# Optimization experiments

Measured on AMD Instinct MI355X. Metric: run time of the kernel, lower is better.

## Reference

```python
import jax, jax.numpy as jnp
import numpy as np

N, F_IN, D_OUT, H = 8192, 512, 64, 8
ALPHA = 0.2
NEG_INF = jnp.float32(-9e15)


def setup_inputs() -> dict:
    key = jax.random.key(0)
    k1, k2, k3, k4, k5 = jax.random.split(key, 5)
    x = jax.random.normal(k1, (N, F_IN), dtype=jnp.float32)
    # sparse-ish binary adjacency (avg degree ~33) with self-loops, stored dense
    adj = (jax.random.uniform(k2, (N, N)) < 0.004).astype(jnp.float32)
    adj = jnp.maximum(adj, jnp.eye(N, dtype=jnp.float32))
    W = jax.random.normal(k3, (H, F_IN, D_OUT), dtype=jnp.float32) * 0.05
    a1 = jax.random.normal(k4, (H, D_OUT), dtype=jnp.float32) * 0.05
    a2 = jax.random.normal(k5, (H, D_OUT), dtype=jnp.float32) * 0.05
    return {"x": x, "adj": adj, "W": W, "a1": a1, "a2": a2}


def reference(x, adj, W, a1, a2):
    mask = adj > 0
    outputs = []
    for h in range(H):  # fixed small head count (matches original per-head loop)
        Wh = x @ W[h]                      # [N, D]
        f1 = Wh @ a1[h]                    # [N]
        f2 = Wh @ a2[h]                    # [N]
        e = jax.nn.leaky_relu(f1[:, None] + f2[None, :], ALPHA)  # [N, N]
        att = jnp.where(mask, e, NEG_INF)
        att = jax.nn.softmax(att, axis=1)  # dropout omitted (eval mode)
        outputs.append(att @ Wh)           # [N, D]
    return jnp.concatenate(outputs, axis=1)  # [N, H*D]
```

## Files before the change

kernel.cpp:

```cpp
#include <hip/hip_runtime.h>
#include <hip/hip_bf16.h>
#include <cstdint>

#define N_NODES 8192
#define F_IN    512
#define D_O     64
#define H_N     8
#define NOUT    512
#define MAXD    128

#define BM 64
#define BN 128
#define BK 64

typedef __attribute__((ext_vector_type(8))) short short8;
typedef __attribute__((ext_vector_type(4))) float f32x4;

static __device__ __forceinline__ ushort f2bf(float f) {
  union { float f; uint32_t u; } v; v.f = f;
  uint32_t r = v.u + 0x7FFFu + ((v.u >> 16) & 1u);
  return (ushort)(r >> 16);
}
static __device__ __forceinline__ float bf2f(ushort u) {
  union { uint32_t u; float f; } v; v.u = ((uint32_t)u) << 16;
  return v.f;
}

__global__ __launch_bounds__(256) void convert(const float* __restrict__ x,
                                               const float* __restrict__ W,
                                               ushort* __restrict__ xb,
                                               ushort* __restrict__ Wt) {
  __shared__ float Ws[64][65];
  const int b = blockIdx.x, t = threadIdx.x;
  if (b < 2048) {
    const int gid = b * 256 + t;
    #pragma unroll
    for (int it = 0; it < 2; ++it) {
      const int q = gid + it * 524288;
      const float4 v = ((const float4*)x)[q];
      ushort4 u;
      u.x = f2bf(v.x); u.y = f2bf(v.y); u.z = f2bf(v.z); u.w = f2bf(v.w);
      ((ushort4*)xb)[q] = u;
    }
  } else {
    const int bb = b - 2048;
    const int h = bb >> 3, kt = bb & 7;
    const int d = t & 63, krg = (t >> 6) * 16;
    const float* src = &W[((size_t)h * F_IN + kt * 64 + krg) * D_O + d];
    #pragma unroll
    for (int q = 0; q < 16; ++q)
      Ws[krg + q][d] = src[(size_t)q * D_O];
    __syncthreads();
    const int d0 = t >> 2, kq = (t & 3) * 16;
    ushort* dst = &Wt[(size_t)h * D_O * F_IN + (size_t)d0 * F_IN + kt * 64 + kq];
    #pragma unroll
    for (int q = 0; q < 16; ++q)
      dst[q] = f2bf(Ws[kq + q][d0]);
  }
}

__global__ __launch_bounds__(256) void scan_gemm(const uint32_t* __restrict__ adj,
                                                 const ushort* __restrict__ xb,
                                                 const ushort* __restrict__ Wt,
                                                 const float* __restrict__ a1,
                                                 const float* __restrict__ a2,
                                                 ushort* __restrict__ Whb,
                                                 float* __restrict__ f1,
                                                 float* __restrict__ f2,
                                                 int* __restrict__ nbr_g,
                                                 int* __restrict__ deg_g) {
  __shared__ ushort As[BM][BK + 8];
  __shared__ ushort Bs[BN][BK + 8];
  __shared__ int wsum[4];

  const int id   = blockIdx.x;
  const int tid  = threadIdx.x;
  const int lane = tid & 63;
  const int wv   = tid >> 6;

  if (id < 512) {
    const int wr = wv >> 1, wc = wv & 1;
    const int r0 = (id >> 2) * BM;
    const int c0 = (id & 3) * BN;
    const int lm = lane & 15;
    const int lg = lane >> 4;

    f32x4 acc[2][4];
    #pragma unroll
    for (int m2 = 0; m2 < 2; ++m2)
      #pragma unroll
      for (int n2 = 0; n2 < 4; ++n2)
        acc[m2][n2] = (f32x4){0.f, 0.f, 0.f, 0.f};

    for (int k0 = 0; k0 < F_IN; k0 += BK) {
      __syncthreads();
      #pragma unroll
      for (int p = 0; p < 2; ++p) {
        const int e = p * 256 + tid;
        const int row = e >> 3, ck = (e & 7) * 8;
        *(short8*)&As[row][ck] = *(const short8*)&xb[(size_t)(r0 + row) * F_IN + k0 + ck];
      }
      #pragma unroll
      for (int p = 0; p < 4; ++p) {
        const int e = p * 256 + tid;
        const int row = e >> 3, ck = (e & 7) * 8;
        *(short8*)&Bs[row][ck] = *(const short8*)&Wt[(size_t)(c0 + row) * F_IN + k0 + ck];
      }
      __syncthreads();

      #pragma unroll
      for (int kk = 0; kk < 2; ++kk) {
        const int koff = kk * 32 + lg * 8;
        short8 af[2], bf[4];
        #pragma unroll
        for (int m2 = 0; m2 < 2; ++m2)
          af[m2] = *(const short8*)&As[wr * 32 + m2 * 16 + lm][koff];
        #pragma unroll
        for (int n2 = 0; n2 < 4; ++n2)
          bf[n2] = *(const short8*)&Bs[wc * 64 + n2 * 16 + lm][koff];
        #pragma unroll
        for (int m2 = 0; m2 < 2; ++m2)
          #pragma unroll
          for (int n2 = 0; n2 < 4; ++n2)
            acc[m2][n2] = __builtin_amdgcn_mfma_f32_16x16x32_bf16(af[m2], bf[n2], acc[m2][n2], 0, 0, 0);
      }
    }

    const int head = (c0 >> 6) + wc;
    float a1v[4], a2v[4];
    #pragma unroll
    for (int n2 = 0; n2 < 4; ++n2) {
      a1v[n2] = a1[head * D_O + n2 * 16 + lm];
      a2v[n2] = a2[head * D_O + n2 * 16 + lm];
    }
    #pragma unroll
    for (int m2 = 0; m2 < 2; ++m2) {
      #pragma unroll
      for (int r = 0; r < 4; ++r) {
        const int row = r0 + wr * 32 + m2 * 16 + lg * 4 + r;
        float p1 = 0.f, p2 = 0.f;
        #pragma unroll
        for (int n2 = 0; n2 < 4; ++n2) {
          const float v = acc[m2][n2][r];
          p1 += v * a1v[n2];
          p2 += v * a2v[n2];
          Whb[(size_t)row * NOUT + c0 + wc * 64 + n2 * 16 + lm] = f2bf(v);
        }
        #pragma unroll
        for (int o = 1; o < 16; o <<= 1) {
          p1 += __shfl_xor(p1, o);
          p2 += __shfl_xor(p2, o);
        }
        if (lm == 0) {
          f1[(size_t)row * H_N + head] = p1;
          f2[(size_t)row * H_N + head] = p2;
        }
      }
    }
  } else {
    const int i = id - 512;
    const uint32_t* arow = adj + (size_t)i * N_NODES;
    uint32_t bits = 0;
    #pragma unroll
    for (int u = 0; u < 8; ++u) {
      const uint4 a = *(const uint4*)&arow[(u * 256 + tid) * 4];
      if (a.x) bits |= 1u << (u * 4 + 0);
      if (a.y) bits |= 1u << (u * 4 + 1);
      if (a.z) bits |= 1u << (u * 4 + 2);
      if (a.w) bits |= 1u << (u * 4 + 3);
    }
    const int cnt = __popc(bits);
    int v = cnt;
    #pragma unroll
    for (int o = 1; o < 64; o <<= 1) {
      int u = __shfl_up(v, o);
      if (lane >= o) v += u;
    }
    if (lane == 63) wsum[wv] = v;
    __syncthreads();
    int base = 0, total = 0;
    #pragma unroll
    for (int ww = 0; ww < 4; ++ww) {
      int s = wsum[ww];
      if (ww < wv) base += s;
      total += s;
    }
    int off = base + v - cnt;
    #pragma unroll
    for (int u = 0; u < 8; ++u)
      #pragma unroll
      for (int bq = 0; bq < 4; ++bq)
        if (bits & (1u << (u * 4 + bq))) {
          if (off < MAXD) nbr_g[(size_t)i * MAXD + off] = (u * 256 + tid) * 4 + bq;
          ++off;
        }
    if (tid == 0) deg_g[i] = min(total, MAXD);
  }
}

__global__ __launch_bounds__(64) void gat_panel(const int* __restrict__ nbr_g,
                                                const int* __restrict__ deg_g,
                                                const ushort* __restrict__ Whb,
                                                const float* __restrict__ f1,
                                                const float* __restrict__ f2,
                                                float* __restrict__ out) {
  const int bid = blockIdx.x;
  const int P   = bid >> 13;
  const int i   = bid & 8191;
  const int t   = threadIdx.x;

  __shared__ int   nbr[MAXD];
  __shared__ float ff[MAXD][2];
  __shared__ float ps[MAXD][2];
  __shared__ float f1s2[2], invs2[2];

  const int deg = deg_g[i];
  if (t < deg)      nbr[t]      = nbr_g[(size_t)i * MAXD + t];
  if (t + 64 < deg) nbr[t + 64] = nbr_g[(size_t)i * MAXD + t + 64];
  if (t < 2) f1s2[t] = f1[(size_t)i * H_N + 2 * P + t];
  __syncthreads();

  for (int n = t; n < deg; n += 64) {
    const float2 v = *(const float2*)&f2[(size_t)nbr[n] * H_N + 2 * P];
    ff[n][0] = v.x; ff[n][1] = v.y;
  }
  __syncthreads();

  {
    const int h = t >> 5;
    const int l = t & 31;
    const float f1v = f1s2[h];
    float m = -3.0e38f;
    for (int n = l; n < deg; n += 32) {
      float e = f1v + ff[n][h];
      e = e > 0.f ? e : 0.2f * e;
      ps[n][h] = e;
      m = fmaxf(m, e);
    }
    #pragma unroll
    for (int o = 16; o; o >>= 1) m = fmaxf(m, __shfl_xor(m, o));
    float s = 0.f;
    for (int n = l; n < deg; n += 32) {
      const float e = __expf(ps[n][h] - m);
      ps[n][h] = e;
      s += e;
    }
    #pragma unroll
    for (int o = 16; o; o >>= 1) s += __shfl_xor(s, o);
    if (l == 0) invs2[h] = 1.0f / s;
  }
  __syncthreads();

  const int ht      = t >> 5;
  const int colbase = P * 128 + t * 2;
  float a0 = 0.f, a1c = 0.f;
  #pragma unroll 8
  for (int n = 0; n < deg; ++n) {
    const float pv = ps[n][ht];
    const ushort2 u = *(const ushort2*)&Whb[(size_t)nbr[n] * NOUT + colbase];
    a0  += pv * bf2f(u.x);
    a1c += pv * bf2f(u.y);
  }
  const float inv = invs2[ht];
  float2 o2; o2.x = a0 * inv; o2.y = a1c * inv;
  *(float2*)&out[(size_t)i * NOUT + colbase] = o2;
}

extern "C" void kernel_launch(void* const* d_in, const int* in_sizes, int n_in,
                              void* d_out, int out_size, void* d_ws, size_t ws_size,
                              hipStream_t stream) {
  const float* x   = (const float*)d_in[0];
  const float* adj = (const float*)d_in[1];
  const float* W   = (const float*)d_in[2];
  const float* a1  = (const float*)d_in[3];
  const float* a2  = (const float*)d_in[4];
  float* out = (float*)d_out;

  ushort* Whb = (ushort*)d_ws;
  ushort* xb  = Whb + (size_t)N_NODES * NOUT;
  ushort* Wt  = xb + (size_t)N_NODES * F_IN;
  float*  f1  = (float*)(Wt + (size_t)H_N * D_O * F_IN);
  float*  f2  = f1 + (size_t)N_NODES * H_N;
  int*    nbr_g = (int*)(f2 + (size_t)N_NODES * H_N);
  int*    deg_g = nbr_g + (size_t)N_NODES * MAXD;

  hipLaunchKernelGGL(convert, dim3(2112), dim3(256), 0, stream, x, W, xb, Wt);
  hipLaunchKernelGGL(scan_gemm, dim3(512 + N_NODES), dim3(256), 0, stream,
                     (const uint32_t*)adj, xb, Wt, a1, a2, Whb, f1, f2, nbr_g, deg_g);
  hipLaunchKernelGGL(gat_panel, dim3(4 * N_NODES), dim3(64), 0, stream,
                     nbr_g, deg_g, Whb, f1, f2, out);
}
```

Baseline: 94.06 us.

## Fuse x bf16 conversion into GEMM, split scan kernel, pack two rows per panel block

The standalone conversion of x to bf16 is removed. The GEMM now loads fp32 x tiles and converts them while staging into shared memory, which avoids writing and re-reading an 8 MB bf16 copy. The fused scan/GEMM kernel is split into separate scan and GEMM launches, adding one launch. The aggregation kernel now processes two rows per 128-thread block instead of one row per 64-thread block, halving the block count at the cost of some extra LDS per block.

After: 96.52 us. 2.6% more time.

```diff
diff --git a/kernel.cpp b/kernel.cpp
--- a/kernel.cpp
+++ b/kernel.cpp
@@ -26,228 +26,220 @@
   return v.f;
 }
 
-__global__ __launch_bounds__(256) void convert(const float* __restrict__ x,
-                                               const float* __restrict__ W,
-                                               ushort* __restrict__ xb,
-                                               ushort* __restrict__ Wt) {
+__global__ __launch_bounds__(256) void convert_wt(const float* __restrict__ W,
+                                                  ushort* __restrict__ Wt) {
   __shared__ float Ws[64][65];
-  const int b = blockIdx.x, t = threadIdx.x;
-  if (b < 2048) {
-    const int gid = b * 256 + t;
-    #pragma unroll
-    for (int it = 0; it < 2; ++it) {
-      const int q = gid + it * 524288;
-      const float4 v = ((const float4*)x)[q];
-      ushort4 u;
-      u.x = f2bf(v.x); u.y = f2bf(v.y); u.z = f2bf(v.z); u.w = f2bf(v.w);
-      ((ushort4*)xb)[q] = u;
-    }
-  } else {
-    const int bb = b - 2048;
-    const int h = bb >> 3, kt = bb & 7;
-    const int d = t & 63, krg = (t >> 6) * 16;
-    const float* src = &W[((size_t)h * F_IN + kt * 64 + krg) * D_O + d];
-    #pragma unroll
-    for (int q = 0; q < 16; ++q)
-      Ws[krg + q][d] = src[(size_t)q * D_O];
-    __syncthreads();
-    const int d0 = t >> 2, kq = (t & 3) * 16;
-    ushort* dst = &Wt[(size_t)h * D_O * F_IN + (size_t)d0 * F_IN + kt * 64 + kq];
-    #pragma unroll
-    for (int q = 0; q < 16; ++q)
-      dst[q] = f2bf(Ws[kq + q][d0]);
-  }
-}
-
-__global__ __launch_bounds__(256) void scan_gemm(const uint32_t* __restrict__ adj,
-                                                 const ushort* __restrict__ xb,
-                                                 const ushort* __restrict__ Wt,
-                                                 const float* __restrict__ a1,
-                                                 const float* __restrict__ a2,
-                                                 ushort* __restrict__ Whb,
-                                                 float* __restrict__ f1,
-                                                 float* __restrict__ f2,
-                                                 int* __restrict__ nbr_g,
-                                                 int* __restrict__ deg_g) {
-  __shared__ ushort As[BM][BK + 8];
-  __shared__ ushort Bs[BN][BK + 8];
+  const int bb = blockIdx.x;
+  const int t  = threadIdx.x;
+  const int h = bb >> 3, kt = bb & 7;
+  const int d = t & 63, krg = (t >> 6) * 16;
+  const float* src = &W[((size_t)h * F_IN + kt * 64 + krg) * D_O + d];
+  #pragma unroll
+  for (int q = 0; q < 16; ++q)
+    Ws[krg + q][d] = src[(size_t)q * D_O];
+  __syncthreads();
+  const int d0 = t >> 2, kq = (t & 3) * 16;
+  ushort* dst = &Wt[(size_t)h * D_O * F_IN + (size_t)d0 * F_IN + kt * 64 + kq];
+  #pragma unroll
+  for (int q = 0; q < 16; ++q)
+    dst[q] = f2bf(Ws[kq + q][d0]);
+}
+
+__global__ __launch_bounds__(256) void scan(const uint32_t* __restrict__ adj,
+                                            int* __restrict__ nbr_g,
+                                            int* __restrict__ deg_g) {
   __shared__ int wsum[4];
-
-  const int id   = blockIdx.x;
+  const int i    = blockIdx.x;
   const int tid  = threadIdx.x;
   const int lane = tid & 63;
   const int wv   = tid >> 6;
 
-  if (id < 512) {
-    const int wr = wv >> 1, wc = wv & 1;
-    const int r0 = (id >> 2) * BM;
-    const int c0 = (id & 3) * BN;
-    const int lm = lane & 15;
-    const int lg = lane >> 4;
-
-    f32x4 acc[2][4];
-    #pragma unroll
-    for (int m2 = 0; m2 < 2; ++m2)
+  const uint32_t* arow = adj + (size_t)i * N_NODES;
+  uint32_t bits = 0;
+  #pragma unroll
+  for (int u = 0; u < 8; ++u) {
+    const uint4 a = *(const uint4*)&arow[(u * 256 + tid) * 4];
+    if (a.x) bits |= 1u << (u * 4 + 0);
+    if (a.y) bits |= 1u << (u * 4 + 1);
+    if (a.z) bits |= 1u << (u * 4 + 2);
+    if (a.w) bits |= 1u << (u * 4 + 3);
+  }
+  const int cnt = __popc(bits);
+  int v = cnt;
+  #pragma unroll
+  for (int o = 1; o < 64; o <<= 1) {
+    int u = __shfl_up(v, o);
+    if (lane >= o) v += u;
+  }
+  if (lane == 63) wsum[wv] = v;
+  __syncthreads();
+  int base = 0, total = 0;
+  #pragma unroll
+  for (int ww = 0; ww < 4; ++ww) {
+    int s = wsum[ww];
+    if (ww < wv) base += s;
+    total += s;
+  }
+  int off = base + v - cnt;
+  #pragma unroll
+  for (int u = 0; u < 8; ++u)
+    #pragma unroll
+    for (int bq = 0; bq < 4; ++bq)
+      if (bits & (1u << (u * 4 + bq))) {
+        if (off < MAXD) nbr_g[(size_t)i * MAXD + off] = (u * 256 + tid) * 4 + bq;
+        ++off;
+      }
+  if (tid == 0) deg_g[i] = min(total, MAXD);
+}
+
+__global__ __launch_bounds__(256) void gemm_f(const float* __restrict__ x,
+                                              const ushort* __restrict__ Wt,
+                                              const float* __restrict__ a1,
+                                              const float* __restrict__ a2,
+                                              ushort* __restrict__ Whb,
+                                              float* __restrict__ f1,
+                                              float* __restrict__ f2) {
+  __shared__ ushort As[BM][BK + 8];
+  __shared__ ushort Bs[BN][BK + 8];
+
+  const int tid  = threadIdx.x;
+  const int lane = tid & 63;
+  const int wv   = tid >> 6;
+  const int wr   = wv >> 1, wc = wv & 1;
+  const int r0   = blockIdx.y * BM;
+  const int c0   = blockIdx.x * BN;
+  const int lm   = lane & 15;
+  const int lg   = lane >> 4;
+
+  f32x4 acc[2][4];
+  #pragma unroll
+  for (int m2 = 0; m2 < 2; ++m2)
+    #pragma unroll
+    for (int n2 = 0; n2 < 4; ++n2)
+      acc[m2][n2] = (f32x4){0.f, 0.f, 0.f, 0.f};
+
+  for (int k0 = 0; k0 < F_IN; k0 += BK) {
+    __syncthreads();
+    #pragma unroll
+    for (int p = 0; p < 4; ++p) {
+      const int e = p * 256 + tid;
+      const int row = e >> 4, q4 = (e & 15) * 4;
+      const float4 v = *(const float4*)&x[(size_t)(r0 + row) * F_IN + k0 + q4];
+      ushort4 u;
+      u.x = f2bf(v.x); u.y = f2bf(v.y); u.z = f2bf(v.z); u.w = f2bf(v.w);
+      *(ushort4*)&As[row][q4] = u;
+    }
+    #pragma unroll
+    for (int p = 0; p < 4; ++p) {
+      const int e = p * 256 + tid;
+      const int row = e >> 3, ck = (e & 7) * 8;
+      *(short8*)&Bs[row][ck] = *(const short8*)&Wt[(size_t)(c0 + row) * F_IN + k0 + ck];
+    }
+    __syncthreads();
+
+    #pragma unroll
+    for (int kk = 0; kk < 2; ++kk) {
+      const int koff = kk * 32 + lg * 8;
+      short8 af[2], bf[4];
+      #pragma unroll
+      for (int m2 = 0; m2 < 2; ++m2)
+        af[m2] = *(const short8*)&As[wr * 32 + m2 * 16 + lm][koff];
       #pragma unroll
       for (int n2 = 0; n2 < 4; ++n2)
-        acc[m2][n2] = (f32x4){0.f, 0.f, 0.f, 0.f};
-
-    for (int k0 = 0; k0 < F_IN; k0 += BK) {
-      __syncthreads();
-      #pragma unroll
-      for (int p = 0; p < 2; ++p) {
-        const int e = p * 256 + tid;
-        const int row = e >> 3, ck = (e & 7) * 8;
-        *(short8*)&As[row][ck] = *(const short8*)&xb[(size_t)(r0 + row) * F_IN + k0 + ck];
-      }
-      #pragma unroll
-      for (int p = 0; p < 4; ++p) {
-        const int e = p * 256 + tid;
-        const int row = e >> 3, ck = (e & 7) * 8;
-        *(short8*)&Bs[row][ck] = *(const short8*)&Wt[(size_t)(c0 + row) * F_IN + k0 + ck];
-      }
-      __syncthreads();
-
-      #pragma unroll
-      for (int kk = 0; kk < 2; ++kk) {
-        const int koff = kk * 32 + lg * 8;
-        short8 af[2], bf[4];
-        #pragma unroll
-        for (int m2 = 0; m2 < 2; ++m2)
-          af[m2] = *(const short8*)&As[wr * 32 + m2 * 16 + lm][koff];
+        bf[n2] = *(const short8*)&Bs[wc * 64 + n2 * 16 + lm][koff];
+      #pragma unroll
+      for (int m2 = 0; m2 < 2; ++m2)
         #pragma unroll
         for (int n2 = 0; n2 < 4; ++n2)
-          bf[n2] = *(const short8*)&Bs[wc * 64 + n2 * 16 + lm][koff];
-        #pragma unroll
-        for (int m2 = 0; m2 < 2; ++m2)
-          #pragma unroll
-          for (int n2 = 0; n2 < 4; ++n2)
-            acc[m2][n2] = __builtin_amdgcn_mfma_f32_16x16x32_bf16(af[m2], bf[n2], acc[m2][n2], 0, 0, 0);
-      }
-    }
-
-    const int head = (c0 >> 6) + wc;
-    float a1v[4], a2v[4];
-    #pragma unroll
-    for (int n2 = 0; n2 < 4; ++n2) {
-      a1v[n2] = a1[head * D_O + n2 * 16 + lm];
-      a2v[n2] = a2[head * D_O + n2 * 16 + lm];
-    }
-    #pragma unroll
-    for (int m2 = 0; m2 < 2; ++m2) {
-      #pragma unroll
-      for (int r = 0; r < 4; ++r) {
-        const int row = r0 + wr * 32 + m2 * 16 + lg * 4 + r;
-        float p1 = 0.f, p2 = 0.f;
-        #pragma unroll
-        for (int n2 = 0; n2 < 4; ++n2) {
-          const float v = acc[m2][n2][r];
-          p1 += v * a1v[n2];
-          p2 += v * a2v[n2];
-          Whb[(size_t)row * NOUT + c0 + wc * 64 + n2 * 16 + lm] = f2bf(v);
-        }
-        #pragma unroll
-        for (int o = 1; o < 16; o <<= 1) {
-          p1 += __shfl_xor(p1, o);
-          p2 += __shfl_xor(p2, o);
-        }
-        if (lm == 0) {
-          f1[(size_t)row * H_N + head] = p1;
-          f2[(size_t)row * H_N + head] = p2;
-        }
-      }
-    }
-  } else {
-    const int i = id - 512;
-    const uint32_t* arow = adj + (size_t)i * N_NODES;
-    uint32_t bits = 0;
-    #pragma unroll
-    for (int u = 0; u < 8; ++u) {
-      const uint4 a = *(const uint4*)&arow[(u * 256 + tid) * 4];
-      if (a.x) bits |= 1u << (u * 4 + 0);
-      if (a.y) bits |= 1u << (u * 4 + 1);
-      if (a.z) bits |= 1u << (u * 4 + 2);
-      if (a.w) bits |= 1u << (u * 4 + 3);
-    }
-    const int cnt = __popc(bits);
-    int v = cnt;
-    #pragma unroll
-    for (int o = 1; o < 64; o <<= 1) {
-      int u = __shfl_up(v, o);
-      if (lane >= o) v += u;
-    }
-    if (lane == 63) wsum[wv] = v;
-    __syncthreads();
-    int base = 0, total = 0;
-    #pragma unroll
-    for (int ww = 0; ww < 4; ++ww) {
-      int s = wsum[ww];
-      if (ww < wv) base += s;
-      total += s;
-    }
-    int off = base + v - cnt;
-    #pragma unroll
-    for (int u = 0; u < 8; ++u)
-      #pragma unroll
-      for (int bq = 0; bq < 4; ++bq)
-        if (bits & (1u << (u * 4 + bq))) {
-          if (off < MAXD) nbr_g[(size_t)i * MAXD + off] = (u * 256 + tid) * 4 + bq;
-          ++off;
-        }
-    if (tid == 0) deg_g[i] = min(total, MAXD);
-  }
-}
-
-__global__ __launch_bounds__(64) void gat_panel(const int* __restrict__ nbr_g,
-                                                const int* __restrict__ deg_g,
-                                                const ushort* __restrict__ Whb,
-                                                const float* __restrict__ f1,
-                                                const float* __restrict__ f2,
-                                                float* __restrict__ out) {
+          acc[m2][n2] = __builtin_amdgcn_mfma_f32_16x16x32_bf16(af[m2], bf[n2], acc[m2][n2], 0, 0, 0);
+    }
+  }
+
+  const int head = (c0 >> 6) + wc;
+  float a1v[4], a2v[4];
+  #pragma unroll
+  for (int n2 = 0; n2 < 4; ++n2) {
+    a1v[n2] = a1[head * D_O + n2 * 16 + lm];
+    a2v[n2] = a2[head * D_O + n2 * 16 + lm];
+  }
+  #pragma unroll
+  for (int m2 = 0; m2 < 2; ++m2) {
+    #pragma unroll
+    for (int r = 0; r < 4; ++r) {
+      const int row = r0 + wr * 32 + m2 * 16 + lg * 4 + r;
+      float p1 = 0.f, p2 = 0.f;
+      #pragma unroll
+      for (int n2 = 0; n2 < 4; ++n2) {
+        const float v = acc[m2][n2][r];
+        p1 += v * a1v[n2];
+        p2 += v * a2v[n2];
+        Whb[(size_t)row * NOUT + c0 + wc * 64 + n2 * 16 + lm] = f2bf(v);
+      }
+      #pragma unroll
+      for (int o = 1; o < 16; o <<= 1) {
+        p1 += __shfl_xor(p1, o);
+        p2 += __shfl_xor(p2, o);
+      }
+      if (lm == 0) {
+        f1[(size_t)row * H_N + head] = p1;
+        f2[(size_t)row * H_N + head] = p2;
+      }
+    }
+  }
+}
+
+__global__ __launch_bounds__(128) void gat_panel(const int* __restrict__ nbr_g,
+                                                 const int* __restrict__ deg_g,
+                                                 const ushort* __restrict__ Whb,
+                                                 const float* __restrict__ f1,
+                                                 const float* __restrict__ f2,
+                                                 float* __restrict__ out) {
   const int bid = blockIdx.x;
-  const int P   = bid >> 13;
-  const int i   = bid & 8191;
-  const int t   = threadIdx.x;
-
-  __shared__ int   nbr[MAXD];
-  __shared__ float ff[MAXD][2];
-  __shared__ float ps[MAXD][2];
-  __shared__ float f1s2[2], invs2[2];
+  const int P   = bid >> 12;
+  const int rp  = bid & 4095;
+  const int w   = threadIdx.x >> 6;
+  const int i   = rp * 2 + w;
+  const int t   = threadIdx.x & 63;
+
+  __shared__ int   nbr[2][MAXD];
+  __shared__ float ff[2][MAXD][2];
+  __shared__ float ps[2][MAXD][2];
+  __shared__ float f1s2[2][2], invs2[2][2];
 
   const int deg = deg_g[i];
-  if (t < deg)      nbr[t]      = nbr_g[(size_t)i * MAXD + t];
-  if (t + 64 < deg) nbr[t + 64] = nbr_g[(size_t)i * MAXD + t + 64];
-  if (t < 2) f1s2[t] = f1[(size_t)i * H_N + 2 * P + t];
+  if (t < deg)      nbr[w][t]      = nbr_g[(size_t)i * MAXD + t];
+  if (t + 64 < deg) nbr[w][t + 64] = nbr_g[(size_t)i * MAXD + t + 64];
+  if (t < 2) f1s2[w][t] = f1[(size_t)i * H_N + 2 * P + t];
   __syncthreads();
 
   for (int n = t; n < deg; n += 64) {
-    const float2 v = *(const float2*)&f2[(size_t)nbr[n] * H_N + 2 * P];
-    ff[n][0] = v.x; ff[n][1] = v.y;
+    const float2 v = *(const float2*)&f2[(size_t)nbr[w][n] * H_N + 2 * P];
+    ff[w][n][0] = v.x; ff[w][n][1] = v.y;
   }
   __syncthreads();
 
   {
     const int h = t >> 5;
     const int l = t & 31;
-    const float f1v = f1s2[h];
+    const float f1v = f1s2[w][h];
     float m = -3.0e38f;
     for (int n = l; n < deg; n += 32) {
-      float e = f1v + ff[n][h];
+      float e = f1v + ff[w][n][h];
       e = e > 0.f ? e : 0.2f * e;
-      ps[n][h] = e;
+      ps[w][n][h] = e;
       m = fmaxf(m, e);
     }
     #pragma unroll
     for (int o = 16; o; o >>= 1) m = fmaxf(m, __shfl_xor(m, o));
     float s = 0.f;
     for (int n = l; n < deg; n += 32) {
-      const float e = __expf(ps[n][h] - m);
-      ps[n][h] = e;
+      const float e = __expf(ps[w][n][h] - m);
+      ps[w][n][h] = e;
       s += e;
     }
     #pragma unroll
     for (int o = 16; o; o >>= 1) s += __shfl_xor(s, o);
-    if (l == 0) invs2[h] = 1.0f / s;
+    if (l == 0) invs2[w][h] = 1.0f / s;
   }
   __syncthreads();
 
@@ -256,12 +248,12 @@
   float a0 = 0.f, a1c = 0.f;
   #pragma unroll 8
   for (int n = 0; n < deg; ++n) {
-    const float pv = ps[n][ht];
-    const ushort2 u = *(const ushort2*)&Whb[(size_t)nbr[n] * NOUT + colbase];
+    const float pv = ps[w][n][ht];
+    const ushort2 u = *(const ushort2*)&Whb[(size_t)nbr[w][n] * NOUT + colbase];
     a0  += pv * bf2f(u.x);
     a1c += pv * bf2f(u.y);
   }
-  const float inv = invs2[ht];
+  const float inv = invs2[w][ht];
   float2 o2; o2.x = a0 * inv; o2.y = a1c * inv;
   *(float2*)&out[(size_t)i * NOUT + colbase] = o2;
 }
@@ -277,16 +269,17 @@
   float* out = (float*)d_out;
 
   ushort* Whb = (ushort*)d_ws;
-  ushort* xb  = Whb + (size_t)N_NODES * NOUT;
-  ushort* Wt  = xb + (size_t)N_NODES * F_IN;
+  ushort* Wt  = Whb + (size_t)N_NODES * NOUT;
   float*  f1  = (float*)(Wt + (size_t)H_N * D_O * F_IN);
   float*  f2  = f1 + (size_t)N_NODES * H_N;
   int*    nbr_g = (int*)(f2 + (size_t)N_NODES * H_N);
   int*    deg_g = nbr_g + (size_t)N_NODES * MAXD;
 
-  hipLaunchKernelGGL(convert, dim3(2112), dim3(256), 0, stream, x, W, xb, Wt);
-  hipLaunchKernelGGL(scan_gemm, dim3(512 + N_NODES), dim3(256), 0, stream,
-                     (const uint32_t*)adj, xb, Wt, a1, a2, Whb, f1, f2, nbr_g, deg_g);
-  hipLaunchKernelGGL(gat_panel, dim3(4 * N_NODES), dim3(64), 0, stream,
+  hipLaunchKernelGGL(convert_wt, dim3(64), dim3(256), 0, stream, W, Wt);
+  hipLaunchKernelGGL(scan, dim3(N_NODES), dim3(256), 0, stream,
+                     (const uint32_t*)adj, nbr_g, deg_g);
+  hipLaunchKernelGGL(gemm_f, dim3(NOUT / BN, N_NODES / BM), dim3(256), 0, stream,
+                     x, Wt, a1, a2, Whb, f1, f2);
+  hipLaunchKernelGGL(gat_panel, dim3(4 * N_NODES / 2), dim3(128), 0, stream,
                      nbr_g, deg_g, Whb, f1, f2, out);
 }
```

## Fuse x bf16 conversion into GEMM, merge adj scan with W convert, shrink nbr to ushort

Applied to the files above, without the earlier changes.

Drops the separate x-to-bf16 pass and its 8 MB round trip by converting x on the fly while loading A tiles in a new GEMM kernel. That kernel uses 512 threads, a 32-row tile covering all 512 output columns and a K step of 32. The adjacency scan now shares a launch with the W transpose/convert instead of the GEMM, and neighbor indices are stored as ushort to halve their traffic. The trade-off is that the GEMM now runs after the scan rather than overlapping with it, and the smaller K tile means more syncs per block.

Result: slower. 96.87 us (+3.0%).

```diff
diff --git a/kernel.cpp b/kernel.cpp
--- a/kernel.cpp
+++ b/kernel.cpp
@@ -9,9 +9,8 @@
 #define NOUT    512
 #define MAXD    128
 
-#define BM 64
-#define BN 128
-#define BK 64
+#define BM 32
+#define BK 32
 
 typedef __attribute__((ext_vector_type(8))) short short8;
 typedef __attribute__((ext_vector_type(4))) float f32x4;
@@ -26,140 +25,20 @@
   return v.f;
 }
 
-__global__ __launch_bounds__(256) void convert(const float* __restrict__ x,
-                                               const float* __restrict__ W,
-                                               ushort* __restrict__ xb,
-                                               ushort* __restrict__ Wt) {
+__global__ __launch_bounds__(256) void scan_cvt(const uint32_t* __restrict__ adj,
+                                                const float* __restrict__ W,
+                                                ushort* __restrict__ Wt,
+                                                ushort* __restrict__ nbr_g,
+                                                int* __restrict__ deg_g) {
   __shared__ float Ws[64][65];
-  const int b = blockIdx.x, t = threadIdx.x;
-  if (b < 2048) {
-    const int gid = b * 256 + t;
-    #pragma unroll
-    for (int it = 0; it < 2; ++it) {
-      const int q = gid + it * 524288;
-      const float4 v = ((const float4*)x)[q];
-      ushort4 u;
-      u.x = f2bf(v.x); u.y = f2bf(v.y); u.z = f2bf(v.z); u.w = f2bf(v.w);
-      ((ushort4*)xb)[q] = u;
-    }
-  } else {
-    const int bb = b - 2048;
-    const int h = bb >> 3, kt = bb & 7;
-    const int d = t & 63, krg = (t >> 6) * 16;
-    const float* src = &W[((size_t)h * F_IN + kt * 64 + krg) * D_O + d];
-    #pragma unroll
-    for (int q = 0; q < 16; ++q)
-      Ws[krg + q][d] = src[(size_t)q * D_O];
-    __syncthreads();
-    const int d0 = t >> 2, kq = (t & 3) * 16;
-    ushort* dst = &Wt[(size_t)h * D_O * F_IN + (size_t)d0 * F_IN + kt * 64 + kq];
-    #pragma unroll
-    for (int q = 0; q < 16; ++q)
-      dst[q] = f2bf(Ws[kq + q][d0]);
-  }
-}
-
-__global__ __launch_bounds__(256) void scan_gemm(const uint32_t* __restrict__ adj,
-                                                 const ushort* __restrict__ xb,
-                                                 const ushort* __restrict__ Wt,
-                                                 const float* __restrict__ a1,
-                                                 const float* __restrict__ a2,
-                                                 ushort* __restrict__ Whb,
-                                                 float* __restrict__ f1,
-                                                 float* __restrict__ f2,
-                                                 int* __restrict__ nbr_g,
-                                                 int* __restrict__ deg_g) {
-  __shared__ ushort As[BM][BK + 8];
-  __shared__ ushort Bs[BN][BK + 8];
   __shared__ int wsum[4];
-
-  const int id   = blockIdx.x;
-  const int tid  = threadIdx.x;
-  const int lane = tid & 63;
-  const int wv   = tid >> 6;
-
-  if (id < 512) {
-    const int wr = wv >> 1, wc = wv & 1;
-    const int r0 = (id >> 2) * BM;
-    const int c0 = (id & 3) * BN;
-    const int lm = lane & 15;
-    const int lg = lane >> 4;
-
-    f32x4 acc[2][4];
-    #pragma unroll
-    for (int m2 = 0; m2 < 2; ++m2)
-      #pragma unroll
-      for (int n2 = 0; n2 < 4; ++n2)
-        acc[m2][n2] = (f32x4){0.f, 0.f, 0.f, 0.f};
-
-    for (int k0 = 0; k0 < F_IN; k0 += BK) {
-      __syncthreads();
-      #pragma unroll
-      for (int p = 0; p < 2; ++p) {
-        const int e = p * 256 + tid;
-        const int row = e >> 3, ck = (e & 7) * 8;
-        *(short8*)&As[row][ck] = *(const short8*)&xb[(size_t)(r0 + row) * F_IN + k0 + ck];
-      }
-      #pragma unroll
-      for (int p = 0; p < 4; ++p) {
-        const int e = p * 256 + tid;
-        const int row = e >> 3, ck = (e & 7) * 8;
-        *(short8*)&Bs[row][ck] = *(const short8*)&Wt[(size_t)(c0 + row) * F_IN + k0 + ck];
-      }
-      __syncthreads();
-
-      #pragma unroll
-      for (int kk = 0; kk < 2; ++kk) {
-        const int koff = kk * 32 + lg * 8;
-        short8 af[2], bf[4];
-        #pragma unroll
-        for (int m2 = 0; m2 < 2; ++m2)
-          af[m2] = *(const short8*)&As[wr * 32 + m2 * 16 + lm][koff];
-        #pragma unroll
-        for (int n2 = 0; n2 < 4; ++n2)
-          bf[n2] = *(const short8*)&Bs[wc * 64 + n2 * 16 + lm][koff];
-        #pragma unroll
-        for (int m2 = 0; m2 < 2; ++m2)
-          #pragma unroll
-          for (int n2 = 0; n2 < 4; ++n2)
-            acc[m2][n2] = __builtin_amdgcn_mfma_f32_16x16x32_bf16(af[m2], bf[n2], acc[m2][n2], 0, 0, 0);
-      }
-    }
-
-    const int head = (c0 >> 6) + wc;
-    float a1v[4], a2v[4];
-    #pragma unroll
-    for (int n2 = 0; n2 < 4; ++n2) {
-      a1v[n2] = a1[head * D_O + n2 * 16 + lm];
-      a2v[n2] = a2[head * D_O + n2 * 16 + lm];
-    }
-    #pragma unroll
-    for (int m2 = 0; m2 < 2; ++m2) {
-      #pragma unroll
-      for (int r = 0; r < 4; ++r) {
-        const int row = r0 + wr * 32 + m2 * 16 + lg * 4 + r;
-        float p1 = 0.f, p2 = 0.f;
-        #pragma unroll
-        for (int n2 = 0; n2 < 4; ++n2) {
-          const float v = acc[m2][n2][r];
-          p1 += v * a1v[n2];
-          p2 += v * a2v[n2];
-          Whb[(size_t)row * NOUT + c0 + wc * 64 + n2 * 16 + lm] = f2bf(v);
-        }
-        #pragma unroll
-        for (int o = 1; o < 16; o <<= 1) {
-          p1 += __shfl_xor(p1, o);
-          p2 += __shfl_xor(p2, o);
-        }
-        if (lm == 0) {
-          f1[(size_t)row * H_N + head] = p1;
-          f2[(size_t)row * H_N + head] = p2;
-        }
-      }
-    }
-  } else {
-    const int i = id - 512;
-    const uint32_t* arow = adj + (size_t)i * N_NODES;
+  const int b   = blockIdx.x;
+  const int tid = threadIdx.x;
+
+  if (b < N_NODES) {
+    const int lane = tid & 63;
+    const int wv   = tid >> 6;
+    const uint32_t* arow = adj + (size_t)b * N_NODES;
     uint32_t bits = 0;
     #pragma unroll
     for (int u = 0; u < 8; ++u) {
@@ -191,14 +70,116 @@
       #pragma unroll
       for (int bq = 0; bq < 4; ++bq)
         if (bits & (1u << (u * 4 + bq))) {
-          if (off < MAXD) nbr_g[(size_t)i * MAXD + off] = (u * 256 + tid) * 4 + bq;
+          if (off < MAXD) nbr_g[(size_t)b * MAXD + off] = (ushort)((u * 256 + tid) * 4 + bq);
           ++off;
         }
-    if (tid == 0) deg_g[i] = min(total, MAXD);
-  }
-}
-
-__global__ __launch_bounds__(64) void gat_panel(const int* __restrict__ nbr_g,
+    if (tid == 0) deg_g[b] = min(total, MAXD);
+  } else {
+    const int bb = b - N_NODES;
+    const int h = bb >> 3, kt = bb & 7;
+    const int d = tid & 63, krg = (tid >> 6) * 16;
+    const float* src = &W[((size_t)h * F_IN + kt * 64 + krg) * D_O + d];
+    #pragma unroll
+    for (int q = 0; q < 16; ++q)
+      Ws[krg + q][d] = src[(size_t)q * D_O];
+    __syncthreads();
+    const int d0 = tid >> 2, kq = (tid & 3) * 16;
+    ushort* dst = &Wt[(size_t)h * D_O * F_IN + (size_t)d0 * F_IN + kt * 64 + kq];
+    #pragma unroll
+    for (int q = 0; q < 16; ++q)
+      dst[q] = f2bf(Ws[kq + q][d0]);
+  }
+}
+
+__global__ __launch_bounds__(512) void gemm_f(const float* __restrict__ x,
+                                              const ushort* __restrict__ Wt,
+                                              const float* __restrict__ a1,
+                                              const float* __restrict__ a2,
+                                              ushort* __restrict__ Whb,
+                                              float* __restrict__ f1,
+                                              float* __restrict__ f2) {
+  __shared__ ushort As[BM][BK + 8];
+  __shared__ ushort Bs[NOUT][BK + 8];
+
+  const int tid  = threadIdx.x;
+  const int lane = tid & 63;
+  const int wc   = tid >> 6;
+  const int r0   = blockIdx.x * BM;
+  const int lm   = lane & 15;
+  const int lg   = lane >> 4;
+
+  f32x4 acc[2][4];
+  #pragma unroll
+  for (int m2 = 0; m2 < 2; ++m2)
+    #pragma unroll
+    for (int n2 = 0; n2 < 4; ++n2)
+      acc[m2][n2] = (f32x4){0.f, 0.f, 0.f, 0.f};
+
+  for (int k0 = 0; k0 < F_IN; k0 += BK) {
+    __syncthreads();
+    {
+      const int row = tid >> 4, q2 = (tid & 15) * 2;
+      const float2 v = *(const float2*)&x[(size_t)(r0 + row) * F_IN + k0 + q2];
+      ushort2 u; u.x = f2bf(v.x); u.y = f2bf(v.y);
+      *(ushort2*)&As[row][q2] = u;
+    }
+    #pragma unroll
+    for (int p = 0; p < 4; ++p) {
+      const int e = p * 512 + tid;
+      const int row = e >> 2, ck = (e & 3) * 8;
+      *(short8*)&Bs[row][ck] = *(const short8*)&Wt[(size_t)row * F_IN + k0 + ck];
+    }
+    __syncthreads();
+
+    const int koff = lg * 8;
+    short8 af[2], bf[4];
+    #pragma unroll
+    for (int m2 = 0; m2 < 2; ++m2)
+      af[m2] = *(const short8*)&As[m2 * 16 + lm][koff];
+    #pragma unroll
+    for (int n2 = 0; n2 < 4; ++n2)
+      bf[n2] = *(const short8*)&Bs[wc * 64 + n2 * 16 + lm][koff];
+    #pragma unroll
+    for (int m2 = 0; m2 < 2; ++m2)
+      #pragma unroll
+      for (int n2 = 0; n2 < 4; ++n2)
+        acc[m2][n2] = __builtin_amdgcn_mfma_f32_16x16x32_bf16(af[m2], bf[n2], acc[m2][n2], 0, 0, 0);
+  }
+
+  const int head = wc;
+  float a1v[4], a2v[4];
+  #pragma unroll
+  for (int n2 = 0; n2 < 4; ++n2) {
+    a1v[n2] = a1[head * D_O + n2 * 16 + lm];
+    a2v[n2] = a2[head * D_O + n2 * 16 + lm];
+  }
+  #pragma unroll
+  for (int m2 = 0; m2 < 2; ++m2) {
+    #pragma unroll
+    for (int r = 0; r < 4; ++r) {
+      const int row = r0 + m2 * 16 + lg * 4 + r;
+      float p1 = 0.f, p2 = 0.f;
+      #pragma unroll
+      for (int n2 = 0; n2 < 4; ++n2) {
+        const float v = acc[m2][n2][r];
+        p1 += v * a1v[n2];
+        p2 += v * a2v[n2];
+        Whb[(size_t)row * NOUT + head * D_O + n2 * 16 + lm] = f2bf(v);
+      }
+      #pragma unroll
+      for (int o = 1; o < 16; o <<= 1) {
+        p1 += __shfl_xor(p1, o);
+        p2 += __shfl_xor(p2, o);
+      }
+      if (lm == 0) {
+        f1[(size_t)row * H_N + head] = p1;
+        f2[(size_t)row * H_N + head] = p2;
+      }
+    }
+  }
+}
+
+__global__ __launch_bounds__(64) void gat_panel(const ushort* __restrict__ nbr_g,
                                                 const int* __restrict__ deg_g,
                                                 const ushort* __restrict__ Whb,
                                                 const float* __restrict__ f1,
@@ -277,16 +258,16 @@
   float* out = (float*)d_out;
 
   ushort* Whb = (ushort*)d_ws;
-  ushort* xb  = Whb + (size_t)N_NODES * NOUT;
-  ushort* Wt  = xb + (size_t)N_NODES * F_IN;
+  ushort* Wt  = Whb + (size_t)N_NODES * NOUT;
   float*  f1  = (float*)(Wt + (size_t)H_N * D_O * F_IN);
   float*  f2  = f1 + (size_t)N_NODES * H_N;
-  int*    nbr_g = (int*)(f2 + (size_t)N_NODES * H_N);
-  int*    deg_g = nbr_g + (size_t)N_NODES * MAXD;
-
-  hipLaunchKernelGGL(convert, dim3(2112), dim3(256), 0, stream, x, W, xb, Wt);
-  hipLaunchKernelGGL(scan_gemm, dim3(512 + N_NODES), dim3(256), 0, stream,
-                     (const uint32_t*)adj, xb, Wt, a1, a2, Whb, f1, f2, nbr_g, deg_g);
+  ushort* nbr_g = (ushort*)(f2 + (size_t)N_NODES * H_N);
+  int*    deg_g = (int*)(nbr_g + (size_t)N_NODES * MAXD);
+
+  hipLaunchKernelGGL(scan_cvt, dim3(N_NODES + 64), dim3(256), 0, stream,
+                     (const uint32_t*)adj, W, Wt, nbr_g, deg_g);
+  hipLaunchKernelGGL(gemm_f, dim3(N_NODES / BM), dim3(512), 0, stream,
+                     x, Wt, a1, a2, Whb, f1, f2);
   hipLaunchKernelGGL(gat_panel, dim3(4 * N_NODES), dim3(64), 0, stream,
                      nbr_g, deg_g, Whb, f1, f2, out);
 }
```
